# Kernel tuning notes

Hardware: AMD Instinct MI355X
Metric: run time of the kernel (lower is better)

Reference implementation:

```python
import jax, jax.numpy as jnp
import numpy as np

H = 512

def setup_inputs() -> dict:
    key = jax.random.key(0)
    ks = jax.random.split(key, 8)
    b, s, m, n, h = 8, 128, 32, 64, H
    sc = 1.0 / np.sqrt(h)
    return {
        "x": jax.random.normal(ks[0], (b, s, m, h), dtype=jnp.float32),
        "y": jax.random.normal(ks[1], (b, s, n, h), dtype=jnp.float32),
        # MultiHeadSelfAtt (additive self-attentive pooling: b*m*h -> b*h)
        "Wa1": jax.random.normal(ks[2], (h, h), dtype=jnp.float32) * sc,
        "ba1": jnp.zeros((h,), dtype=jnp.float32),
        "wa2": jax.random.normal(ks[3], (h,), dtype=jnp.float32) * sc,
        # gate Linear(2h -> h), torch layout weight: (h, 2h)
        "Wl": jax.random.normal(ks[4], (h, 2 * h), dtype=jnp.float32) * (1.0 / np.sqrt(2 * h)),
        "bl": jnp.zeros((h,), dtype=jnp.float32),
    }

def reference(x, y, Wa1, ba1, wa2, Wl, bl):
    h = x.shape[-1]
    # attentive pooling over m for every (b, s) slice: b s m h -> b s h
    scores = jnp.tanh(x @ Wa1 + ba1) @ wa2          # b s m
    attn = jax.nn.softmax(scores, axis=-1)
    pooled = jnp.einsum('bsm,bsmh->bsh', attn, x)   # b s h
    # step i (i>=1) uses pooled x at step i-1
    i_x = pooled[:, :-1]                            # b (s-1) h
    Wy, Wi = Wl[:, :h], Wl[:, h:]                   # split concat-linear
    pre = jnp.einsum('bsnh,gh->bsng', y[:, 1:], Wy) \
        + (i_x @ Wi.T + bl)[:, :, None, :]          # b (s-1) n h
    gate = jax.nn.sigmoid(pre)
    out_rest = y[:, 1:] + i_x[:, :, None, :] * gate
    return jnp.concatenate([y[:, :1], out_rest], axis=1)  # b s n h
```

## Files before the change

### kernel.cpp

```cpp
#include <hip/hip_runtime.h>
#include <cstdint>
#include <cstddef>

#define H 512
#define SEQ 128

typedef __bf16 v8bf __attribute__((ext_vector_type(8)));
typedef float v4f __attribute__((ext_vector_type(4)));
typedef unsigned short v8us __attribute__((ext_vector_type(8)));

__device__ __forceinline__ unsigned short f2bf(float f) {
    unsigned int u = __float_as_uint(f);
    u = (u + 0x7FFFu + ((u >> 16) & 1u)) >> 16;
    return (unsigned short)u;
}
__device__ __forceinline__ float bf2f(unsigned short h) {
    return __uint_as_float(((unsigned int)h) << 16);
}
__device__ __forceinline__ v8bf load_bf8(const unsigned short* p) {
    return *reinterpret_cast<const v8bf*>(p);
}
__device__ __forceinline__ float fast_tanh(float v) {
    float e = __expf(2.f * v);
    return 1.f - 2.f * __builtin_amdgcn_rcpf(e + 1.f);
}
__device__ __forceinline__ float fast_sigmoid(float v) {
    return __builtin_amdgcn_rcpf(1.f + __expf(-v));
}
__device__ __forceinline__ v8us cvt8u(float4 lo, float4 hi) {
    v8us r;
    r[0] = f2bf(lo.x); r[1] = f2bf(lo.y); r[2] = f2bf(lo.z); r[3] = f2bf(lo.w);
    r[4] = f2bf(hi.x); r[5] = f2bf(hi.y); r[6] = f2bf(hi.z); r[7] = f2bf(hi.w);
    return r;
}


__global__ __launch_bounds__(256) void prep_kernel(
        const float* __restrict__ Wa1, const float* __restrict__ Wl,
        unsigned short* __restrict__ WyS, unsigned short* __restrict__ WiS,
        unsigned short* __restrict__ WaS) {
    int tg = blockIdx.x * 256 + threadIdx.x;
    int mat = tg >> 15;
    int idx = tg & 32767;
    int lane = idx & 63;
    int ks = (idx >> 6) & 15;
    int c = idx >> 10;
    int g = c * 16 + (lane & 15);
    int hb = ks * 32 + ((lane >> 4) << 3);
    unsigned short o[8];
    unsigned short* dst;
    if (mat == 0) {
        const float* s = Wl + (size_t)g * 1024 + hb;
#pragma unroll
        for (int j = 0; j < 8; ++j) o[j] = f2bf(s[j]);
        dst = WyS + (size_t)idx * 8;
    } else if (mat == 1) {
        const float* s = Wl + (size_t)g * 1024 + 512 + hb;
#pragma unroll
        for (int j = 0; j < 8; ++j) o[j] = f2bf(s[j]);
        dst = WiS + (size_t)idx * 8;
    } else {
#pragma unroll
        for (int j = 0; j < 8; ++j) o[j] = f2bf(Wa1[(size_t)(hb + j) * H + g]);
        dst = WaS + (size_t)idx * 8;
    }
    *reinterpret_cast<ushort4*>(dst)     = *reinterpret_cast<ushort4*>(&o[0]);
    *reinterpret_cast<ushort4*>(dst + 4) = *reinterpret_cast<ushort4*>(&o[4]);
}

__global__ __launch_bounds__(256, 4) void attn_pool_kernel(
        const float* __restrict__ x, const unsigned short* __restrict__ WaS,
        const float* __restrict__ ba1, const float* __restrict__ wa2,
        float* __restrict__ ixf, unsigned short* __restrict__ ixb) {
    __shared__ __align__(16) unsigned short Xb[32][520];
    __shared__ float attn[32];
    __shared__ float scpart[4][32];

    int bid = blockIdx.x;
    int b = bid / 127, s = bid % 127;
    int t = threadIdx.x;

    const float4* x4 = reinterpret_cast<const float4*>(x + (size_t)(b * SEQ + s) * 32 * H);
#pragma unroll
    for (int i = 0; i < 16; ++i) {
        int idx4 = t + i * 256;
        float4 v = x4[idx4];
        int e = idx4 * 4, m = e >> 9, h = e & 511;
        ushort4 o;
        o.x = f2bf(v.x); o.y = f2bf(v.y); o.z = f2bf(v.z); o.w = f2bf(v.w);
        *reinterpret_cast<ushort4*>(&Xb[m][h]) = o;
    }
    __syncthreads();

    int w = t >> 6, lane = t & 63, q = lane >> 4, c16 = lane & 15;

    v4f acc[2][8];
#pragma unroll
    for (int mi = 0; mi < 2; ++mi)
#pragma unroll
        for (int ci = 0; ci < 8; ++ci) acc[mi][ci] = (v4f){0.f, 0.f, 0.f, 0.f};

    const unsigned short* Bb = WaS + (size_t)(w * 8 * 16) * 512 + lane * 8;

#pragma unroll
    for (int ks = 0; ks < 16; ++ks) {
        v8bf a0 = load_bf8(&Xb[c16][ks * 32 + q * 8]);
        v8bf a1 = load_bf8(&Xb[16 + c16][ks * 32 + q * 8]);
#pragma unroll
        for (int ci = 0; ci < 8; ++ci) {
            v8bf bb = load_bf8(Bb + (size_t)(ci * 16 + ks) * 512);
            acc[0][ci] = __builtin_amdgcn_mfma_f32_16x16x32_bf16(a0, bb, acc[0][ci], 0, 0, 0);
            acc[1][ci] = __builtin_amdgcn_mfma_f32_16x16x32_bf16(a1, bb, acc[1][ci], 0, 0, 0);
        }
    }

    float sr[2][4] = {{0.f, 0.f, 0.f, 0.f}, {0.f, 0.f, 0.f, 0.f}};
#pragma unroll
    for (int ci = 0; ci < 8; ++ci) {
        int g = (w * 8 + ci) * 16 + c16;
        float w2 = wa2[g];
        float bv = ba1[g];
#pragma unroll
        for (int mi = 0; mi < 2; ++mi)
#pragma unroll
            for (int i = 0; i < 4; ++i)
                sr[mi][i] += w2 * fast_tanh(acc[mi][ci][i] + bv);
    }
#pragma unroll
    for (int off = 1; off < 16; off <<= 1) {
#pragma unroll
        for (int mi = 0; mi < 2; ++mi)
#pragma unroll
            for (int i = 0; i < 4; ++i) sr[mi][i] += __shfl_xor(sr[mi][i], off);
    }
    if (c16 == 0) {
#pragma unroll
        for (int mi = 0; mi < 2; ++mi)
#pragma unroll
            for (int i = 0; i < 4; ++i) scpart[w][mi * 16 + q * 4 + i] = sr[mi][i];
    }
    __syncthreads();

    if (t < 64) {
        int m = t & 31;
        float v = scpart[0][m] + scpart[1][m] + scpart[2][m] + scpart[3][m];
        float mx = v;
#pragma unroll
        for (int off = 1; off < 32; off <<= 1) mx = fmaxf(mx, __shfl_xor(mx, off));
        float e = __expf(v - mx);
        float sum = e;
#pragma unroll
        for (int off = 1; off < 32; off <<= 1) sum += __shfl_xor(sum, off);
        if (t < 32) attn[m] = e * __builtin_amdgcn_rcpf(sum);
    }
    __syncthreads();

    int h0 = t * 2;
    float p0 = 0.f, p1 = 0.f;
#pragma unroll
    for (int m = 0; m < 32; ++m) {
        float am = attn[m];
        p0 += am * bf2f(Xb[m][h0]);
        p1 += am * bf2f(Xb[m][h0 + 1]);
    }
    size_t r = (size_t)bid;
    ixf[r * H + h0] = p0;
    ixf[r * H + h0 + 1] = p1;
    ixb[r * H + h0] = f2bf(p0);
    ixb[r * H + h0 + 1] = f2bf(p1);
}

__global__ __launch_bounds__(256) void ipre_kernel(
        const unsigned short* __restrict__ ixb, const unsigned short* __restrict__ WiS,
        const float* __restrict__ bl, float* __restrict__ ipre) {
    int row16 = blockIdx.x * 16;
    int t = threadIdx.x, w = t >> 6, lane = t & 63, q = lane >> 4, c16 = lane & 15;
    int c0 = blockIdx.y * 8 + w * 2;

    v4f acc0 = {0.f, 0.f, 0.f, 0.f};
    v4f acc1 = {0.f, 0.f, 0.f, 0.f};
    const unsigned short* arow = ixb + (size_t)(row16 + c16) * H + q * 8;
#pragma unroll
    for (int ks = 0; ks < 16; ++ks) {
        v8bf a = load_bf8(arow + ks * 32);
        acc0 = __builtin_amdgcn_mfma_f32_16x16x32_bf16(
            a, load_bf8(WiS + (size_t)(c0 * 16 + ks) * 512 + lane * 8), acc0, 0, 0, 0);
        acc1 = __builtin_amdgcn_mfma_f32_16x16x32_bf16(
            a, load_bf8(WiS + (size_t)((c0 + 1) * 16 + ks) * 512 + lane * 8), acc1, 0, 0, 0);
    }
#pragma unroll
    for (int cc = 0; cc < 2; ++cc) {
        int g = (c0 + cc) * 16 + c16;
        float blv = bl[g];
        v4f a = cc ? acc1 : acc0;
#pragma unroll
        for (int i = 0; i < 4; ++i) {
            int row = row16 + q * 4 + i;
            if (row < 1016) ipre[(size_t)row * H + g] = a[i] + blv;
        }
    }
}

__global__ __launch_bounds__(512, 4) void main_kernel(
        const float* __restrict__ y, const unsigned short* __restrict__ WyS,
        const float* __restrict__ ixf, const float* __restrict__ ipre,
        float* __restrict__ out) {
    int bid0 = blockIdx.x;
    int t = threadIdx.x;

    if (bid0 >= 1016) {
        int cb = bid0 - 1016;
        int b = cb >> 1, half = cb & 1;
        size_t base = ((size_t)(b * SEQ)) * 64 * H + (size_t)half * 32 * H;
        const float4* y4 = reinterpret_cast<const float4*>(y + base);
        float4* o4 = reinterpret_cast<float4*>(out + base);
#pragma unroll
        for (int i = 0; i < 8; ++i) o4[t + i * 512] = y4[t + i * 512];
        return;
    }

    int bid = (bid0 & 7) * 127 + (bid0 >> 3);

    int rg = bid >> 1;
    int ch = bid & 1;

    __shared__ __align__(16) char arena[57344];
    unsigned short* Ab = (unsigned short*)arena;
    unsigned short* Bbuf = (unsigned short*)(arena + 20480);
    float* ip_s = (float*)(arena + 53248);
    float* ix_s = (float*)(arena + 55296);
    float* ep   = (float*)arena;

    int t0 = rg * 2;

    int arow  = t >> 2;
    int acol0 = (t & 3) * 8;
    int atid  = t0 + (arow >> 6);
    int ab    = atid / 127, asm1 = atid % 127;
    const float* yrow = y + ((size_t)(ab * SEQ + asm1 + 1) * 64 + (arow & 63)) * H;

    int w = t >> 6, lane = t & 63, q = lane >> 4, c16 = lane & 15;
    int ck0 = w * 2;
    const unsigned short* bsrc0 = WyS + (size_t)((ch * 16 + ck0) * 16) * 512 + lane * 8;
    const unsigned short* bsrc1 = WyS + (size_t)((ch * 16 + ck0 + 1) * 16) * 512 + lane * 8;

    {
        int tile = t >> 8, gl = t & 255;
        size_t rrow = (size_t)(t0 + tile) * H + ch * 256 + gl;
        ip_s[t] = ipre[rrow];
        ix_s[t] = ixf[rrow];
    }

    float4 a_lo[2], a_hi[2]; v8us b0r[2], b1r[2];

    {
        float4 a0 = *reinterpret_cast<const float4*>(yrow + acol0);
        float4 a1 = *reinterpret_cast<const float4*>(yrow + acol0 + 4);
        v8us b0 = *reinterpret_cast<const v8us*>(bsrc0);
        v8us b1 = *reinterpret_cast<const v8us*>(bsrc1);
        a_lo[1] = *reinterpret_cast<const float4*>(yrow + 32 + acol0);
        a_hi[1] = *reinterpret_cast<const float4*>(yrow + 32 + acol0 + 4);
        b0r[1] = *reinterpret_cast<const v8us*>(bsrc0 + 512);
        b1r[1] = *reinterpret_cast<const v8us*>(bsrc1 + 512);
        *reinterpret_cast<v8us*>(&Ab[arow * 40 + acol0]) = cvt8u(a0, a1);
        *reinterpret_cast<v8us*>(&Bbuf[ck0 * 512 + lane * 8]) = b0;
        *reinterpret_cast<v8us*>(&Bbuf[(ck0 + 1) * 512 + lane * 8]) = b1;
    }
    __syncthreads();

    int wr = w >> 1;
    int wc = w & 1;

    v4f acc[2][8];
#pragma unroll
    for (int rt = 0; rt < 2; ++rt)
#pragma unroll
        for (int ci = 0; ci < 8; ++ci) acc[rt][ci] = (v4f){0.f, 0.f, 0.f, 0.f};

#pragma unroll
    for (int p = 0; p < 16; ++p) {
        const int cur = p & 1;
        const int nxt = cur ^ 1;
        if (p < 14) {
            a_lo[cur] = *reinterpret_cast<const float4*>(yrow + (p + 2) * 32 + acol0);
            a_hi[cur] = *reinterpret_cast<const float4*>(yrow + (p + 2) * 32 + acol0 + 4);
            b0r[cur] = *reinterpret_cast<const v8us*>(bsrc0 + (p + 2) * 512);
            b1r[cur] = *reinterpret_cast<const v8us*>(bsrc1 + (p + 2) * 512);
        }
        if (p < 15) {
            *reinterpret_cast<v8us*>(&Ab[nxt * 5120 + arow * 40 + acol0]) =
                cvt8u(a_lo[nxt], a_hi[nxt]);
            *reinterpret_cast<v8us*>(&Bbuf[nxt * 8192 + ck0 * 512 + lane * 8]) = b0r[nxt];
            *reinterpret_cast<v8us*>(&Bbuf[nxt * 8192 + (ck0 + 1) * 512 + lane * 8]) = b1r[nxt];
        }

        v8bf af0 = load_bf8(&Ab[cur * 5120 + (wr * 32 + c16) * 40 + q * 8]);
        v8bf af1 = load_bf8(&Ab[cur * 5120 + (wr * 32 + 16 + c16) * 40 + q * 8]);
#pragma unroll
        for (int ci = 0; ci < 8; ++ci) {
            v8bf bf = load_bf8(&Bbuf[cur * 8192 + (wc * 8 + ci) * 512 + lane * 8]);
            acc[0][ci] = __builtin_amdgcn_mfma_f32_16x16x32_bf16(af0, bf, acc[0][ci], 0, 0, 0);
            acc[1][ci] = __builtin_amdgcn_mfma_f32_16x16x32_bf16(af1, bf, acc[1][ci], 0, 0, 0);
        }

        if (p < 15) __syncthreads();
    }

    int tile = wr >> 1;
    size_t obase0 = ((size_t)((t0 / 127) * SEQ + t0 % 127 + 1) * 64) * H;
    size_t obase1 = ((size_t)(((t0 + 1) / 127) * SEQ + (t0 + 1) % 127 + 1) * 64) * H;

#pragma unroll
    for (int slab = 0; slab < 4; ++slab) {
        __syncthreads();
        if (wr == slab) {
#pragma unroll
            for (int ci = 0; ci < 8; ++ci) {
                int gl = wc * 128 + ci * 16 + c16;
                float ip = ip_s[tile * 256 + gl];
                float ixv = ix_s[tile * 256 + gl];
#pragma unroll
                for (int rt = 0; rt < 2; ++rt)
#pragma unroll
                    for (int i = 0; i < 4; ++i) {
                        int rl = rt * 16 + q * 4 + i;
                        ep[rl * 260 + gl] = ixv * fast_sigmoid(acc[rt][ci][i] + ip);
                    }
            }
        }
        __syncthreads();
#pragma unroll
        for (int k = 0; k < 4; ++k) {
            int c = t + k * 512;
            int rl = c >> 6;
            int cx = (c & 63) * 4;
            int browg = slab * 32 + rl;
            int tl = browg >> 6;
            int n = browg & 63;
            size_t off = (tl ? obase1 : obase0) + (size_t)n * H + ch * 256 + cx;
            float4 g4 = *reinterpret_cast<const float4*>(&ep[rl * 260 + cx]);
            float4 y4 = *reinterpret_cast<const float4*>(&y[off]);
            float4 o;
            o.x = y4.x + g4.x; o.y = y4.y + g4.y;
            o.z = y4.z + g4.z; o.w = y4.w + g4.w;
            *reinterpret_cast<float4*>(&out[off]) = o;
        }
    }
}

extern "C" void kernel_launch(void* const* d_in, const int* in_sizes, int n_in,
                              void* d_out, int out_size, void* d_ws, size_t ws_size,
                              hipStream_t stream) {
    const float* x   = (const float*)d_in[0];
    const float* y   = (const float*)d_in[1];
    const float* Wa1 = (const float*)d_in[2];
    const float* ba1 = (const float*)d_in[3];
    const float* wa2 = (const float*)d_in[4];
    const float* Wl  = (const float*)d_in[5];
    const float* bl  = (const float*)d_in[6];
    float* out = (float*)d_out;

    char* ws = (char*)d_ws;
    unsigned short* WyS  = (unsigned short*)(ws);
    unsigned short* WiS  = (unsigned short*)(ws + 524288);
    unsigned short* WaS  = (unsigned short*)(ws + 1048576);
    float*          ixf  = (float*)(ws + 1572864);
    unsigned short* ixb  = (unsigned short*)(ws + 3670016);
    float*          ipre = (float*)(ws + 4718592);

    hipLaunchKernelGGL(prep_kernel, dim3(384), dim3(256), 0, stream, Wa1, Wl, WyS, WiS, WaS);
    hipLaunchKernelGGL(attn_pool_kernel, dim3(1016), dim3(256), 0, stream,
                       x, WaS, ba1, wa2, ixf, ixb);
    hipLaunchKernelGGL(ipre_kernel, dim3(64, 4), dim3(256), 0, stream, ixb, WiS, bl, ipre);
    hipLaunchKernelGGL(main_kernel, dim3(1032), dim3(512), 0, stream,
                       y, WyS, ixf, ipre, out);
}
```

Measured before the change: 146.4 us.

## Pool two slices per block and trim main kernel LDS for occupancy

The attention pooling kernel now handles two (b,s) slices per block, so each Wa1 B-fragment loaded from global memory feeds twice as many MFMAs, and the grid is halved. The main kernel's A-tile row pitch drops from 40 to 36 halves and the ip/ix staging arrays move out of shared memory into registers loaded just before the epilogue. Together these shrink LDS use so launch bounds can target 6 blocks per CU. The trade-off is more registers in the pooling kernel (double accumulators), fewer pooling blocks, and a possible change in LDS bank conflicts from the new pitch.

```diff
diff --git a/kernel.cpp b/kernel.cpp
--- a/kernel.cpp
+++ b/kernel.cpp
@@ -68,82 +68,112 @@
     *reinterpret_cast<ushort4*>(dst + 4) = *reinterpret_cast<ushort4*>(&o[4]);
 }
 
-__global__ __launch_bounds__(256, 4) void attn_pool_kernel(
+__global__ __launch_bounds__(256, 2) void attn_pool_kernel(
         const float* __restrict__ x, const unsigned short* __restrict__ WaS,
         const float* __restrict__ ba1, const float* __restrict__ wa2,
         float* __restrict__ ixf, unsigned short* __restrict__ ixb) {
-    __shared__ __align__(16) unsigned short Xb[32][520];
-    __shared__ float attn[32];
-    __shared__ float scpart[4][32];
+    __shared__ __align__(16) unsigned short Xb[2][32][520];
+    __shared__ float attn_s[64];
+    __shared__ float scpart[4][64];
 
     int bid = blockIdx.x;
-    int b = bid / 127, s = bid % 127;
     int t = threadIdx.x;
 
-    const float4* x4 = reinterpret_cast<const float4*>(x + (size_t)(b * SEQ + s) * 32 * H);
-#pragma unroll
-    for (int i = 0; i < 16; ++i) {
-        int idx4 = t + i * 256;
-        float4 v = x4[idx4];
-        int e = idx4 * 4, m = e >> 9, h = e & 511;
-        ushort4 o;
-        o.x = f2bf(v.x); o.y = f2bf(v.y); o.z = f2bf(v.z); o.w = f2bf(v.w);
-        *reinterpret_cast<ushort4*>(&Xb[m][h]) = o;
+#pragma unroll
+    for (int tt = 0; tt < 2; ++tt) {
+        int tile = bid * 2 + tt;
+        int b = tile / 127, s = tile % 127;
+        const float4* x4 = reinterpret_cast<const float4*>(
+            x + (size_t)(b * SEQ + s) * 32 * H);
+#pragma unroll
+        for (int i = 0; i < 16; ++i) {
+            int idx4 = t + i * 256;
+            float4 v = x4[idx4];
+            int e = idx4 * 4, m = e >> 9, h = e & 511;
+            ushort4 o;
+            o.x = f2bf(v.x); o.y = f2bf(v.y); o.z = f2bf(v.z); o.w = f2bf(v.w);
+            *reinterpret_cast<ushort4*>(&Xb[tt][m][h]) = o;
+        }
     }
     __syncthreads();
 
     int w = t >> 6, lane = t & 63, q = lane >> 4, c16 = lane & 15;
 
-    v4f acc[2][8];
-#pragma unroll
-    for (int mi = 0; mi < 2; ++mi)
-#pragma unroll
-        for (int ci = 0; ci < 8; ++ci) acc[mi][ci] = (v4f){0.f, 0.f, 0.f, 0.f};
+    v4f acc[2][2][8];
+#pragma unroll
+    for (int tt = 0; tt < 2; ++tt)
+#pragma unroll
+        for (int mi = 0; mi < 2; ++mi)
+#pragma unroll
+            for (int ci = 0; ci < 8; ++ci) acc[tt][mi][ci] = (v4f){0.f, 0.f, 0.f, 0.f};
 
     const unsigned short* Bb = WaS + (size_t)(w * 8 * 16) * 512 + lane * 8;
 
 #pragma unroll
     for (int ks = 0; ks < 16; ++ks) {
-        v8bf a0 = load_bf8(&Xb[c16][ks * 32 + q * 8]);
-        v8bf a1 = load_bf8(&Xb[16 + c16][ks * 32 + q * 8]);
+        v8bf a[2][2];
+#pragma unroll
+        for (int tt = 0; tt < 2; ++tt)
+#pragma unroll
+            for (int mi = 0; mi < 2; ++mi)
+                a[tt][mi] = load_bf8(&Xb[tt][mi * 16 + c16][ks * 32 + q * 8]);
 #pragma unroll
         for (int ci = 0; ci < 8; ++ci) {
             v8bf bb = load_bf8(Bb + (size_t)(ci * 16 + ks) * 512);
-            acc[0][ci] = __builtin_amdgcn_mfma_f32_16x16x32_bf16(a0, bb, acc[0][ci], 0, 0, 0);
-            acc[1][ci] = __builtin_amdgcn_mfma_f32_16x16x32_bf16(a1, bb, acc[1][ci], 0, 0, 0);
-        }
-    }
-
-    float sr[2][4] = {{0.f, 0.f, 0.f, 0.f}, {0.f, 0.f, 0.f, 0.f}};
+#pragma unroll
+            for (int tt = 0; tt < 2; ++tt)
+#pragma unroll
+                for (int mi = 0; mi < 2; ++mi)
+                    acc[tt][mi][ci] = __builtin_amdgcn_mfma_f32_16x16x32_bf16(
+                        a[tt][mi], bb, acc[tt][mi][ci], 0, 0, 0);
+        }
+    }
+
+    float sr[2][2][4];
+#pragma unroll
+    for (int tt = 0; tt < 2; ++tt)
+#pragma unroll
+        for (int mi = 0; mi < 2; ++mi)
+#pragma unroll
+            for (int i = 0; i < 4; ++i) sr[tt][mi][i] = 0.f;
+
 #pragma unroll
     for (int ci = 0; ci < 8; ++ci) {
         int g = (w * 8 + ci) * 16 + c16;
         float w2 = wa2[g];
         float bv = ba1[g];
 #pragma unroll
-        for (int mi = 0; mi < 2; ++mi)
-#pragma unroll
-            for (int i = 0; i < 4; ++i)
-                sr[mi][i] += w2 * fast_tanh(acc[mi][ci][i] + bv);
+        for (int tt = 0; tt < 2; ++tt)
+#pragma unroll
+            for (int mi = 0; mi < 2; ++mi)
+#pragma unroll
+                for (int i = 0; i < 4; ++i)
+                    sr[tt][mi][i] += w2 * fast_tanh(acc[tt][mi][ci][i] + bv);
     }
 #pragma unroll
     for (int off = 1; off < 16; off <<= 1) {
 #pragma unroll
-        for (int mi = 0; mi < 2; ++mi)
-#pragma unroll
-            for (int i = 0; i < 4; ++i) sr[mi][i] += __shfl_xor(sr[mi][i], off);
+        for (int tt = 0; tt < 2; ++tt)
+#pragma unroll
+            for (int mi = 0; mi < 2; ++mi)
+#pragma unroll
+                for (int i = 0; i < 4; ++i) sr[tt][mi][i] += __shfl_xor(sr[tt][mi][i], off);
     }
     if (c16 == 0) {
 #pragma unroll
-        for (int mi = 0; mi < 2; ++mi)
-#pragma unroll
-            for (int i = 0; i < 4; ++i) scpart[w][mi * 16 + q * 4 + i] = sr[mi][i];
+        for (int tt = 0; tt < 2; ++tt)
+#pragma unroll
+            for (int mi = 0; mi < 2; ++mi)
+#pragma unroll
+                for (int i = 0; i < 4; ++i)
+                    scpart[w][tt * 32 + mi * 16 + q * 4 + i] = sr[tt][mi][i];
     }
     __syncthreads();
 
     if (t < 64) {
-        int m = t & 31;
-        float v = scpart[0][m] + scpart[1][m] + scpart[2][m] + scpart[3][m];
+        int m = t & 31, tile = t >> 5;
+        int e0 = tile * 32 + m;
+        float v = scpart[0][e0] + scpart[1][e0] + scpart[2][e0] + scpart[3][e0];
         float mx = v;
 #pragma unroll
         for (int off = 1; off < 32; off <<= 1) mx = fmaxf(mx, __shfl_xor(mx, off));
@@ -151,23 +181,26 @@
         float sum = e;
 #pragma unroll
         for (int off = 1; off < 32; off <<= 1) sum += __shfl_xor(sum, off);
-        if (t < 32) attn[m] = e * __builtin_amdgcn_rcpf(sum);
+        attn_s[e0] = e * __builtin_amdgcn_rcpf(sum);
     }
     __syncthreads();
 
     int h0 = t * 2;
-    float p0 = 0.f, p1 = 0.f;
-#pragma unroll
-    for (int m = 0; m < 32; ++m) {
-        float am = attn[m];
-        p0 += am * bf2f(Xb[m][h0]);
-        p1 += am * bf2f(Xb[m][h0 + 1]);
-    }
-    size_t r = (size_t)bid;
-    ixf[r * H + h0] = p0;
-    ixf[r * H + h0 + 1] = p1;
-    ixb[r * H + h0] = f2bf(p0);
-    ixb[r * H + h0 + 1] = f2bf(p1);
+#pragma unroll
+    for (int tt = 0; tt < 2; ++tt) {
+        float p0 = 0.f, p1 = 0.f;
+#pragma unroll
+        for (int m = 0; m < 32; ++m) {
+            float am = attn_s[tt * 32 + m];
+            p0 += am * bf2f(Xb[tt][m][h0]);
+            p1 += am * bf2f(Xb[tt][m][h0 + 1]);
+        }
+        size_t r = (size_t)(bid * 2 + tt);
+        ixf[r * H + h0] = p0;
+        ixf[r * H + h0 + 1] = p1;
+        ixb[r * H + h0] = f2bf(p0);
+        ixb[r * H + h0 + 1] = f2bf(p1);
+    }
 }
 
 __global__ __launch_bounds__(256) void ipre_kernel(
@@ -201,7 +234,7 @@
     }
 }
 
-__global__ __launch_bounds__(512, 4) void main_kernel(
+__global__ __launch_bounds__(512, 6) void main_kernel(
         const float* __restrict__ y, const unsigned short* __restrict__ WyS,
         const float* __restrict__ ixf, const float* __restrict__ ipre,
         float* __restrict__ out) {
@@ -224,12 +257,10 @@
     int rg = bid >> 1;
     int ch = bid & 1;
 
-    __shared__ __align__(16) char arena[57344];
+    __shared__ __align__(16) char arena[51200];
     unsigned short* Ab = (unsigned short*)arena;
-    unsigned short* Bbuf = (unsigned short*)(arena + 20480);
-    float* ip_s = (float*)(arena + 53248);
-    float* ix_s = (float*)(arena + 55296);
-    float* ep   = (float*)arena;
+    unsigned short* Bbuf = (unsigned short*)(arena + 18432);
+    float* ep = (float*)arena;
 
     int t0 = rg * 2;
 
@@ -243,13 +274,6 @@
     int ck0 = w * 2;
     const unsigned short* bsrc0 = WyS + (size_t)((ch * 16 + ck0) * 16) * 512 + lane * 8;
     const unsigned short* bsrc1 = WyS + (size_t)((ch * 16 + ck0 + 1) * 16) * 512 + lane * 8;
-
-    {
-        int tile = t >> 8, gl = t & 255;
-        size_t rrow = (size_t)(t0 + tile) * H + ch * 256 + gl;
-        ip_s[t] = ipre[rrow];
-        ix_s[t] = ixf[rrow];
-    }
 
     float4 a_lo[2], a_hi[2]; v8us b0r[2], b1r[2];
 
@@ -262,7 +286,7 @@
         a_hi[1] = *reinterpret_cast<const float4*>(yrow + 32 + acol0 + 4);
         b0r[1] = *reinterpret_cast<const v8us*>(bsrc0 + 512);
         b1r[1] = *reinterpret_cast<const v8us*>(bsrc1 + 512);
-        *reinterpret_cast<v8us*>(&Ab[arow * 40 + acol0]) = cvt8u(a0, a1);
+        *reinterpret_cast<v8us*>(&Ab[arow * 36 + acol0]) = cvt8u(a0, a1);
         *reinterpret_cast<v8us*>(&Bbuf[ck0 * 512 + lane * 8]) = b0;
         *reinterpret_cast<v8us*>(&Bbuf[(ck0 + 1) * 512 + lane * 8]) = b1;
     }
@@ -288,14 +312,14 @@
             b1r[cur] = *reinterpret_cast<const v8us*>(bsrc1 + (p + 2) * 512);
         }
         if (p < 15) {
-            *reinterpret_cast<v8us*>(&Ab[nxt * 5120 + arow * 40 + acol0]) =
+            *reinterpret_cast<v8us*>(&Ab[nxt * 4608 + arow * 36 + acol0]) =
                 cvt8u(a_lo[nxt], a_hi[nxt]);
             *reinterpret_cast<v8us*>(&Bbuf[nxt * 8192 + ck0 * 512 + lane * 8]) = b0r[nxt];
             *reinterpret_cast<v8us*>(&Bbuf[nxt * 8192 + (ck0 + 1) * 512 + lane * 8]) = b1r[nxt];
         }
 
-        v8bf af0 = load_bf8(&Ab[cur * 5120 + (wr * 32 + c16) * 40 + q * 8]);
-        v8bf af1 = load_bf8(&Ab[cur * 5120 + (wr * 32 + 16 + c16) * 40 + q * 8]);
+        v8bf af0 = load_bf8(&Ab[cur * 4608 + (wr * 32 + c16) * 36 + q * 8]);
+        v8bf af1 = load_bf8(&Ab[cur * 4608 + (wr * 32 + 16 + c16) * 36 + q * 8]);
 #pragma unroll
         for (int ci = 0; ci < 8; ++ci) {
             v8bf bf = load_bf8(&Bbuf[cur * 8192 + (wc * 8 + ci) * 512 + lane * 8]);
@@ -310,6 +334,15 @@
     size_t obase0 = ((size_t)((t0 / 127) * SEQ + t0 % 127 + 1) * 64) * H;
     size_t obase1 = ((size_t)(((t0 + 1) / 127) * SEQ + (t0 + 1) % 127 + 1) * 64) * H;
 
+    float ipr[8], ixr[8];
+#pragma unroll
+    for (int ci = 0; ci < 8; ++ci) {
+        int gl = wc * 128 + ci * 16 + c16;
+        size_t rr = (size_t)(t0 + tile) * H + ch * 256 + gl;
+        ipr[ci] = ipre[rr];
+        ixr[ci] = ixf[rr];
+    }
+
 #pragma unroll
     for (int slab = 0; slab < 4; ++slab) {
         __syncthreads();
@@ -317,14 +350,12 @@
 #pragma unroll
             for (int ci = 0; ci < 8; ++ci) {
                 int gl = wc * 128 + ci * 16 + c16;
-                float ip = ip_s[tile * 256 + gl];
-                float ixv = ix_s[tile * 256 + gl];
 #pragma unroll
                 for (int rt = 0; rt < 2; ++rt)
 #pragma unroll
                     for (int i = 0; i < 4; ++i) {
                         int rl = rt * 16 + q * 4 + i;
-                        ep[rl * 260 + gl] = ixv * fast_sigmoid(acc[rt][ci][i] + ip);
+                        ep[rl * 260 + gl] = ixr[ci] * fast_sigmoid(acc[rt][ci][i] + ipr[ci]);
                     }
             }
         }
@@ -369,7 +400,7 @@
     float*          ipre = (float*)(ws + 4718592);
 
     hipLaunchKernelGGL(prep_kernel, dim3(384), dim3(256), 0, stream, Wa1, Wl, WyS, WiS, WaS);
-    hipLaunchKernelGGL(attn_pool_kernel, dim3(1016), dim3(256), 0, stream,
+    hipLaunchKernelGGL(attn_pool_kernel, dim3(508), dim3(256), 0, stream,
                        x, WaS, ba1, wa2, ixf, ixb);
     hipLaunchKernelGGL(ipre_kernel, dim3(64, 4), dim3(256), 0, stream, ixb, WiS, bl, ipre);
     hipLaunchKernelGGL(main_kernel, dim3(1032), dim3(512), 0, stream,
```

Measured after the change: 440.8 us. +201.1%, slower.
